# Kernel optimization log

Measured on AMD Instinct MI355X. Metric: run time of the kernel, lower is better.

The kernel has to match this reference:

```python
import jax, jax.numpy as jnp
import numpy as np


def _lstm_cell(x, h, c, Wih, Whh, bih, bhh):
    # PyTorch LSTMCell: gates ordered i, f, g, o
    g = x @ Wih.T + h @ Whh.T + bih + bhh
    H = h.shape[-1]
    i = jax.nn.sigmoid(g[:, :H])
    f = jax.nn.sigmoid(g[:, H:2 * H])
    gg = jnp.tanh(g[:, 2 * H:3 * H])
    o = jax.nn.sigmoid(g[:, 3 * H:])
    c_new = f * c + i * gg
    h_new = o * jnp.tanh(c_new)
    return h_new, c_new


def setup_inputs() -> dict:
    B, S, H = 32, 512, 256
    key = jax.random.key(0)
    ks = jax.random.split(key, 16)
    p = lambda k, shape: jax.random.normal(k, shape, jnp.float32) * 0.05
    return {
        "enc_hidden_states": jax.random.normal(ks[0], (B, S, H), jnp.float32),
        "backward_hidden_state": jax.random.normal(ks[1], (B, H), jnp.float32),
        "backward_cell_state": jax.random.normal(ks[2], (B, H), jnp.float32),
        "attn_W": p(ks[3], (H, 2 * H)),
        "attn_b": p(ks[4], (H,)),
        "attn_V": jax.random.normal(ks[5], (H,), jnp.float32) * 0.1,
        "l1_Wih": p(ks[6], (4 * H, 2 * H)),
        "l1_Whh": p(ks[7], (4 * H, H)),
        "l1_bih": p(ks[8], (4 * H,)),
        "l1_bhh": p(ks[9], (4 * H,)),
        "l2_Wih": p(ks[10], (4 * H, 2 * H)),
        "l2_Whh": p(ks[11], (4 * H, H)),
        "l2_bih": p(ks[12], (4 * H,)),
        "l2_bhh": p(ks[13], (4 * H,)),
        "inp_len": jnp.clip(jax.random.randint(ks[14], (32,), 1, 513), 1, 512).astype(jnp.int32),
    }


def reference(enc_hidden_states, backward_hidden_state, backward_cell_state,
              attn_W, attn_b, attn_V,
              l1_Wih, l1_Whh, l1_bih, l1_bhh,
              l2_Wih, l2_Whh, l2_bih, l2_bhh,
              inp_len):
    B, S, H = enc_hidden_states.shape
    NEG = jnp.float32(-1e9)
    mask = jnp.where(jnp.arange(S)[None, :] < inp_len[:, None], 0.0, NEG)  # (B,S)

    # Linear(cat(q, v)) == q @ Wq.T + v @ Wv.T + b ; hoist out of the time loop.
    Wq, Wv = attn_W[:, :H], attn_W[:, H:]
    pq = enc_hidden_states @ Wq.T                       # (B,S,H)
    pv = enc_hidden_states @ Wv.T + attn_b              # (B,S,H)

    enc_t = jnp.transpose(enc_hidden_states, (1, 0, 2))  # (S,B,H)
    pq_t = jnp.transpose(pq, (1, 0, 2))                   # (S,B,H)

    def step1(carry, xs):
        h, c = carry
        q, pqt = xs
        score = jnp.tanh(pqt[:, None, :] + pv)            # (B,S,H)
        s = jnp.einsum('bsh,h->bs', score, attn_V) + mask
        a = jax.nn.softmax(s, axis=1)
        ctx = jnp.einsum('bs,bsh->bh', a, enc_hidden_states)
        inp = jnp.concatenate([q, ctx], axis=1)           # (B,2H)
        # NOTE: original code passes (decoder_c, decoder_h) i.e. (h=c, c=h) swapped
        h_new, c_new = _lstm_cell(inp, c, h, l1_Wih, l1_Whh, l1_bih, l1_bhh)
        return (h_new, c_new), (h_new, ctx)

    _, (dec_h, ctxs) = jax.lax.scan(step1, (backward_hidden_state, backward_cell_state), (enc_t, pq_t))
    x2 = jnp.concatenate([dec_h, ctxs], axis=2)           # (S,B,2H); dropout = identity (eval)

    # Second layer: packed-sequence LSTM == freeze state and emit zeros past inp_len
    def step2(carry, xs):
        h, c = carry
        x, t = xs
        valid = (t < inp_len)[:, None]
        h_new, c_new = _lstm_cell(x, h, c, l2_Wih, l2_Whh, l2_bih, l2_bhh)
        h2 = jnp.where(valid, h_new, h)
        c2 = jnp.where(valid, c_new, c)
        out = jnp.where(valid, h_new, 0.0)
        return (h2, c2), out

    z = jnp.zeros((B, H), jnp.float32)
    _, out = jax.lax.scan(step2, (z, z), (x2, jnp.arange(S)))
    return jnp.transpose(out, (1, 0, 2))                  # (B,S,H)
```

## Files before the change

### kernel.cpp

```cpp
#include <hip/hip_runtime.h>

typedef _Float16 f16;
typedef _Float16 f16x2 __attribute__((ext_vector_type(2)));
typedef _Float16 f16x8 __attribute__((ext_vector_type(8)));
typedef _Float16 f16x4 __attribute__((ext_vector_type(4)));
typedef float f32x4 __attribute__((ext_vector_type(4)));

#define L2E 1.4426950408889634f
#define K2E 2.8853900817779268f

#define O_PQV   0UL
#define O_GIH2C 0UL
#define O_CTX   33554432UL
#define O_ENCF  41943040UL
#define O_GIH1  50331648UL
#define O_DECT  33554432UL
#define O_WQV   92274688UL
#define O_CPUBT 92274688UL
#define O_H2PT  92340224UL
#define O_W1    92536832UL
#define O_W2    93585408UL
#define O_WHH1  94633984UL
#define O_WHH2  95158272UL
#define O_BQV   95682560UL
#define O_B1    95684608UL
#define O_B2    95688704UL
#define O_V2    95692800UL
#define O_SUMV  95693824UL
#define WS_NEED 95776768UL

__device__ __forceinline__ float fast_sigmoid(float x){
  float e = __builtin_amdgcn_exp2f(-L2E * x);
  return __builtin_amdgcn_rcpf(1.f + e);
}
__device__ __forceinline__ float fast_tanh(float x){
  float e = __builtin_amdgcn_exp2f(K2E * x);
  return 1.f - 2.f * __builtin_amdgcn_rcpf(1.f + e);
}

__device__ __forceinline__ void store_tag(void* p, float a, float b, unsigned tag){
  union { unsigned long long u; unsigned w[2]; } v;
  union { unsigned u; f16 h[2]; } d;
  d.h[0] = (f16)a; d.h[1] = (f16)b;
  v.w[0] = d.u; v.w[1] = tag;
  __hip_atomic_store((unsigned long long*)p, v.u, __ATOMIC_RELAXED, __HIP_MEMORY_SCOPE_AGENT);
}
template<int OFF>
__device__ __forceinline__ int4 ld_i4(const char* p){
  int4 r;
  asm volatile("global_load_dwordx4 %0, %1, off offset:%c2 sc0 sc1"
               : "=v"(r) : "v"(p), "i"(OFF) : "memory");
  return r;
}
__device__ __forceinline__ f16x8 mk_frag(int4 r0, int4 r1){
  union { f16x8 f; int i[4]; } u;
  u.i[0] = r0.x; u.i[1] = r0.z; u.i[2] = r1.x; u.i[3] = r1.z;
  return u.f;
}

__global__ __launch_bounds__(256) void prep_kernel(
    const float* __restrict__ attn_W, const float* __restrict__ attn_b, const float* __restrict__ attn_V,
    const float* __restrict__ l1_Wih, const float* __restrict__ l1_Whh,
    const float* __restrict__ l1_bih, const float* __restrict__ l1_bhh,
    const float* __restrict__ l2_Wih, const float* __restrict__ l2_Whh,
    const float* __restrict__ l2_bih, const float* __restrict__ l2_bhh,
    const float* __restrict__ bcs, char* __restrict__ ws)
{
  long gid = (long)blockIdx.x*256 + threadIdx.x;
  if (gid < 131072){
    int j = (int)(gid >> 8), k = (int)(gid & 255);
    float v = (j < 256) ? attn_W[j*512 + k] : attn_W[(j-256)*512 + 256 + k];
    ((f16*)(ws+O_WQV))[gid] = (f16)(K2E * v);
    return;
  }
  gid -= 131072;
  if (gid < 524288){ ((f16*)(ws+O_W1))[gid] = (f16)l1_Wih[gid]; return; }
  gid -= 524288;
  if (gid < 524288){ ((f16*)(ws+O_W2))[gid] = (f16)l2_Wih[gid]; return; }
  gid -= 524288;
  if (gid < 262144){ ((f16*)(ws+O_WHH1))[gid] = (f16)l1_Whh[gid]; return; }
  gid -= 262144;
  if (gid < 262144){ ((f16*)(ws+O_WHH2))[gid] = (f16)l2_Whh[gid]; return; }
  gid -= 262144;
  if (gid < 512){ ((float*)(ws+O_BQV))[gid] = (gid < 256) ? 0.f : K2E*attn_b[gid-256]; return; }
  gid -= 512;
  if (gid < 1024){ ((float*)(ws+O_B1))[gid] = l1_bih[gid] + l1_bhh[gid]; return; }
  gid -= 1024;
  if (gid < 1024){ ((float*)(ws+O_B2))[gid] = l2_bih[gid] + l2_bhh[gid]; return; }
  gid -= 1024;
  if (gid < 256){ ((float*)(ws+O_V2))[gid] = -2.f*attn_V[gid]; return; }
  gid -= 256;
  if (gid == 0){
    float s = 0.f;
    for (int h=0; h<256; h++) s += attn_V[h];
    *((float*)(ws+O_SUMV)) = s;
  }
}

__global__ __launch_bounds__(256) void encf_kernel(const float* __restrict__ enc, char* __restrict__ ws){
  f16* dst = (f16*)(ws + O_ENCF);
  int i = (blockIdx.x*256 + threadIdx.x)*4;
  float4 v = *(const float4*)(enc + i);
  f16x4 o; o[0] = (f16)v.x; o[1] = (f16)v.y; o[2] = (f16)v.z; o[3] = (f16)v.w;
  *(f16x4*)(dst + i) = o;
}

template<bool CF16>
__global__ __launch_bounds__(256) void gemm_nt(const f16* __restrict__ A0, const f16* __restrict__ A1,
     int K0, const f16* __restrict__ B, int ldb, void* __restrict__ Cp, int ldc,
     int K, const float* __restrict__ bias)
{
  __shared__ f16 As[4096];
  __shared__ f16 Bs[4096];
  const int tid = threadIdx.x;
  const int lane = tid & 63;
  const int wave = tid >> 6;
  const int lm = lane & 15, kg = lane >> 4;
  const int mbase = blockIdx.y * 128;
  const int nbase = blockIdx.x * 128;
  const int wm = (wave >> 1) * 64, wn = (wave & 1) * 64;
  f32x4 acc[4][4];
#pragma unroll
  for (int i=0;i<4;i++)
#pragma unroll
    for (int j=0;j<4;j++) acc[i][j] = 0;
  const int r = tid >> 1, seg = tid & 1;
  for (int kc=0; kc<K; kc+=32){
    const f16* Ap = A0; int kk = kc;
    if (A1 && kc >= K0){ Ap = A1; kk = kc - K0; }
    {
      const f16* srcA = Ap + (size_t)(mbase + r)*256 + kk + seg*16;
      f16x8 va0 = *(const f16x8*)(srcA);
      f16x8 va1 = *(const f16x8*)(srcA + 8);
      *(f16x8*)&As[((seg*2+0)*128 + r)*8] = va0;
      *(f16x8*)&As[((seg*2+1)*128 + r)*8] = va1;
      const f16* srcB = B + (size_t)(nbase + r)*ldb + kc + seg*16;
      f16x8 vb0 = *(const f16x8*)(srcB);
      f16x8 vb1 = *(const f16x8*)(srcB + 8);
      *(f16x8*)&Bs[((seg*2+0)*128 + r)*8] = vb0;
      *(f16x8*)&Bs[((seg*2+1)*128 + r)*8] = vb1;
    }
    __syncthreads();
    f16x8 af[4], bfr[4];
#pragma unroll
    for (int i=0;i<4;i++) af[i]  = *(const f16x8*)&As[(kg*128 + wm + i*16 + lm)*8];
#pragma unroll
    for (int j=0;j<4;j++) bfr[j] = *(const f16x8*)&Bs[(kg*128 + wn + j*16 + lm)*8];
#pragma unroll
    for (int i=0;i<4;i++)
#pragma unroll
      for (int j=0;j<4;j++)
        acc[i][j] = __builtin_amdgcn_mfma_f32_16x16x32_f16(af[i], bfr[j], acc[i][j], 0,0,0);
    __syncthreads();
  }
#pragma unroll
  for (int i=0;i<4;i++){
#pragma unroll
    for (int j=0;j<4;j++){
      int col = nbase + wn + j*16 + lm;
      float bv = bias ? bias[col] : 0.f;
#pragma unroll
      for (int rr=0;rr<4;rr++){
        int row = mbase + wm + i*16 + kg*4 + rr;
        float v = acc[i][j][rr] + bv;
        if (CF16) ((f16*)Cp)[(size_t)row*ldc + col] = (f16)v;
        else      ((float*)Cp)[(size_t)row*ldc + col] = v;
      }
    }
  }
}

__global__ __launch_bounds__(256) void score_ctx_kernel(char* __restrict__ ws,
     const float* __restrict__ enc, const int* __restrict__ inp_len)
{
  __shared__ float s_pq[8][260];
  __shared__ float s_pv[32][260];
  __shared__ float s_sc[8][512];
  __shared__ float s_v2[256];
  __shared__ float s_sv[1];
  const int tid = threadIdx.x;
  const int b = blockIdx.y;
  const int t0 = blockIdx.x * 8;
  const float* pqv = (const float*)(ws + O_PQV);
  f16* ctx = (f16*)(ws + O_CTX);
  const int len = inp_len[b];
  {
    int row = tid >> 5, cb = (tid & 31) * 8;
    const float* src = pqv + (size_t)(b*512 + t0 + row)*512 + cb;
    *(float4*)&s_pq[row][cb]   = *(const float4*)(src);
    *(float4*)&s_pq[row][cb+4] = *(const float4*)(src+4);
    s_v2[tid] = ((const float*)(ws + O_V2))[tid];
    if (tid == 0) s_sv[0] = *((const float*)(ws + O_SUMV));
  }
  const int tt = tid >> 5;
  const int ss2 = tid & 31;
  for (int st=0; st<16; st++){
    {
      int row = tid >> 3, cb = (tid & 7) * 32;
      const float* src = pqv + (size_t)(b*512 + st*32 + row)*512 + 256 + cb;
#pragma unroll
      for (int c=0;c<32;c+=4) *(float4*)&s_pv[row][cb+c] = *(const float4*)(src+c);
    }
    __syncthreads();
    float a0=0.f,a1=0.f,a2=0.f,a3=0.f;
#pragma unroll 8
    for (int h=0;h<256;h+=4){
      float4 q = *(const float4*)&s_pq[tt][h];
      float4 p = *(const float4*)&s_pv[ss2][h];
      float4 w = *(const float4*)&s_v2[h];
      float e0 = __builtin_amdgcn_exp2f(q.x+p.x);
      float e1 = __builtin_amdgcn_exp2f(q.y+p.y);
      float e2 = __builtin_amdgcn_exp2f(q.z+p.z);
      float e3 = __builtin_amdgcn_exp2f(q.w+p.w);
      a0 += w.x * __builtin_amdgcn_rcpf(1.f+e0);
      a1 += w.y * __builtin_amdgcn_rcpf(1.f+e1);
      a2 += w.z * __builtin_amdgcn_rcpf(1.f+e2);
      a3 += w.w * __builtin_amdgcn_rcpf(1.f+e3);
    }
    int s = st*32 + ss2;
    float sc = s_sv[0] + ((a0+a1)+(a2+a3));
    if (s >= len) sc = -1.0e9f;
    s_sc[tt][s] = sc;
    __syncthreads();
  }
  {
    float m = -3.0e38f;
#pragma unroll
    for (int k2=0;k2<16;k2++) m = fmaxf(m, s_sc[tt][ss2 + 32*k2]);
#pragma unroll
    for (int off=16; off>=1; off>>=1) m = fmaxf(m, __shfl_xor(m, off, 64));
    float sum = 0.f;
    float ebuf[16];
#pragma unroll
    for (int k2=0;k2<16;k2++){
      float e = __builtin_amdgcn_exp2f((s_sc[tt][ss2+32*k2] - m) * L2E);
      ebuf[k2] = e; sum += e;
    }
#pragma unroll
    for (int off=16; off>=1; off>>=1) sum += __shfl_xor(sum, off, 64);
    float rinv = __builtin_amdgcn_rcpf(sum);
#pragma unroll
    for (int k2=0;k2<16;k2++) s_sc[tt][ss2+32*k2] = ebuf[k2]*rinv;
  }
  __syncthreads();
  float acc[8] = {0,0,0,0,0,0,0,0};
  const int hg = tid & 31;
  for (int st=0; st<16; st++){
    {
      int row = tid >> 3, cb = (tid & 7)*32;
      const float* src = enc + (size_t)(b*512 + st*32 + row)*256 + cb;
#pragma unroll
      for (int c=0;c<32;c+=4) *(float4*)&s_pv[row][cb+c] = *(const float4*)(src+c);
    }
    __syncthreads();
#pragma unroll 4
    for (int si=0; si<32; si++){
      float a = s_sc[tt][st*32+si];
#pragma unroll
      for (int u=0;u<8;u++) acc[u] += a * s_pv[si][hg + 32*u];
    }
    __syncthreads();
  }
#pragma unroll
  for (int u=0;u<8;u++)
    ctx[(size_t)(b*512 + t0 + tt)*256 + hg + 32*u] = (f16)acc[u];
}

__global__ __launch_bounds__(256) void rec_kernel(char* __restrict__ ws,
        const float* __restrict__ bhs, const float* __restrict__ bcs,
        const int* __restrict__ inp_len, float* __restrict__ out)
{
  __shared__ float s_g[4][32][17];
  __shared__ f16x8 s_buf[2048];
  const int tid = threadIdx.x;
  const int lane = tid & 63;
  const int wave = tid >> 6;
  const int lm = lane & 15;
  const int kg = lane >> 4;
  char* cpubt = ws + O_CPUBT;
  char* h2pt  = ws + O_H2PT;
  char* decpt = ws + O_DECT;
  const int b  = tid >> 3;
  const int kp = tid & 7;
  const int kl0 = kp*2, kl1 = kp*2 + 1;
  const int gslot = wave*256 + lane;
  const int fs = kg*32 + lm;

  if (blockIdx.x < 16) {
    const int isl = blockIdx.x;
    const f16* whh1 = (const f16*)(ws + O_WHH1);
    const f16* gih1 = (const f16*)(ws + O_GIH1);
    f16x8 bf[8];
    {
      int j = wave*256 + isl*16 + lm;
#pragma unroll
      for (int kc=0;kc<8;kc++) bf[kc] = *(const f16x8*)(whh1 + j*256 + kc*32 + kg*8);
    }
    float h0 = bhs[b*256 + isl*16 + kl0];
    float h1 = bhs[b*256 + isl*16 + kl1];
    const int kk0 = isl*16 + kl0;
    const int pu = ((kk0>>5)*128 + ((kk0>>3)&3)*32 + b)*32 + ((kk0&7)>>1)*8;
    store_tag(cpubt + 32768 + pu, bcs[b*256 + kk0], bcs[b*256 + kk0 + 1], 1u);
    for (int t=0;t<512;t++){
      const f16* gp = gih1 + (size_t)(b*512 + t)*1024 + isl*16 + kl0;
      f16x2 gv0 = *(const f16x2*)(gp);
      f16x2 gv1 = *(const f16x2*)(gp+256);
      f16x2 gv2 = *(const f16x2*)(gp+512);
      f16x2 gv3 = *(const f16x2*)(gp+768);
      const char* cb = cpubt + (((t+1)&1)<<15);
      const char* pk0 = cb + (size_t)gslot*32;
      const char* pk2 = pk0 + 4096;
      const unsigned want = (unsigned)(t+1);
      int4 r[8];
      while (true){
        r[0] = ld_i4<0>(pk0);    r[1] = ld_i4<16>(pk0);
        r[2] = ld_i4<2048>(pk0); r[3] = ld_i4<2064>(pk0);
        r[4] = ld_i4<0>(pk2);    r[5] = ld_i4<16>(pk2);
        r[6] = ld_i4<2048>(pk2); r[7] = ld_i4<2064>(pk2);
        asm volatile("s_waitcnt vmcnt(0)" ::: "memory");
        __builtin_amdgcn_sched_barrier(0);
        unsigned mn = 0xFFFFFFFFu;
#pragma unroll
        for (int i=0;i<8;i++){
          unsigned t0 = (unsigned)r[i].y, t1 = (unsigned)r[i].w;
          mn = mn < t0 ? mn : t0;
          mn = mn < t1 ? mn : t1;
        }
        if (__all((int)(mn >= want))) break;
      }
      s_buf[gslot]       = mk_frag(r[0], r[1]);
      s_buf[gslot + 64]  = mk_frag(r[2], r[3]);
      s_buf[gslot + 128] = mk_frag(r[4], r[5]);
      s_buf[gslot + 192] = mk_frag(r[6], r[7]);
      __syncthreads();
      f32x4 acc0 = 0, acc1 = 0;
#pragma unroll
      for (int kc=0;kc<8;kc++){
        f16x8 a0 = s_buf[kc*128 + fs];
        f16x8 a1 = s_buf[kc*128 + fs + 16];
        acc0 = __builtin_amdgcn_mfma_f32_16x16x32_f16(a0, bf[kc], acc0, 0,0,0);
        acc1 = __builtin_amdgcn_mfma_f32_16x16x32_f16(a1, bf[kc], acc1, 0,0,0);
      }
#pragma unroll
      for (int rr=0;rr<4;rr++){
        s_g[wave][kg*4+rr][lm] = acc0[rr];
        s_g[wave][16+kg*4+rr][lm] = acc1[rr];
      }
      __syncthreads();
      {
        float gi0 = s_g[0][b][kl0] + (float)gv0[0];
        float gi1 = s_g[0][b][kl1] + (float)gv0[1];
        float gf0 = s_g[1][b][kl0] + (float)gv1[0];
        float gf1 = s_g[1][b][kl1] + (float)gv1[1];
        float gc0 = s_g[2][b][kl0] + (float)gv2[0];
        float gc1 = s_g[2][b][kl1] + (float)gv2[1];
        float go0 = s_g[3][b][kl0] + (float)gv3[0];
        float go1 = s_g[3][b][kl1] + (float)gv3[1];
        float cn0 = fast_sigmoid(gf0)*h0 + fast_sigmoid(gi0)*fast_tanh(gc0);
        float cn1 = fast_sigmoid(gf1)*h1 + fast_sigmoid(gi1)*fast_tanh(gc1);
        float hn0 = fast_sigmoid(go0)*fast_tanh(cn0);
        float hn1 = fast_sigmoid(go1)*fast_tanh(cn1);
        h0 = hn0; h1 = hn1;
        store_tag(cpubt + ((t&1)<<15) + pu, cn0, cn1, (unsigned)(t+2));
        store_tag(decpt + ((size_t)t<<15) + pu, hn0, hn1, (unsigned)(t+2));
      }
    }
  } else {
    const int isl = blockIdx.x - 16;
    const f16* whh2 = (const f16*)(ws + O_WHH2);
    const f16* w2   = (const f16*)(ws + O_W2);
    const f16* gih2 = (const f16*)(ws + O_GIH2C);
    f16x8 bfh[8], bfx[8];
    {
      int j = wave*256 + isl*16 + lm;
#pragma unroll
      for (int kc=0;kc<8;kc++){
        bfh[kc] = *(const f16x8*)(whh2 + j*256 + kc*32 + kg*8);
        bfx[kc] = *(const f16x8*)(w2 + j*512 + kc*32 + kg*8);
      }
    }
    float c0 = 0.f, c1 = 0.f, hh0 = 0.f, hh1 = 0.f;
    const int lenv = inp_len[b];
    const int kk0 = isl*16 + kl0;
    const int pu = ((kk0>>5)*128 + ((kk0>>3)&3)*32 + b)*32 + ((kk0&7)>>1)*8;
    store_tag(h2pt + 32768 + pu, 0.f, 0.f, 1u);
    for (int t=0;t<512;t++){
      const f16* gp = gih2 + (size_t)(b*512 + t)*1024 + isl*16 + kl0;
      f16x2 gv0 = *(const f16x2*)(gp);
      f16x2 gv1 = *(const f16x2*)(gp+256);
      f16x2 gv2 = *(const f16x2*)(gp+512);
      f16x2 gv3 = *(const f16x2*)(gp+768);
      f32x4 acc0 = 0, acc1 = 0;
      {
        const char* xb = decpt + ((size_t)t<<15);
        const char* px0 = xb + (size_t)gslot*32;
        const char* px2 = px0 + 4096;
        const unsigned wantx = (unsigned)(t+2);
        int4 rx[8];
        while (true){
          rx[0] = ld_i4<0>(px0);    rx[1] = ld_i4<16>(px0);
          rx[2] = ld_i4<2048>(px0); rx[3] = ld_i4<2064>(px0);
          rx[4] = ld_i4<0>(px2);    rx[5] = ld_i4<16>(px2);
          rx[6] = ld_i4<2048>(px2); rx[7] = ld_i4<2064>(px2);
          asm volatile("s_waitcnt vmcnt(0)" ::: "memory");
          __builtin_amdgcn_sched_barrier(0);
          unsigned mn = 0xFFFFFFFFu;
#pragma unroll
          for (int i=0;i<8;i++){
            unsigned a0 = (unsigned)rx[i].y, a1 = (unsigned)rx[i].w;
            mn = mn < a0 ? mn : a0;
            mn = mn < a1 ? mn : a1;
          }
          if (__all((int)(mn >= wantx))) break;
        }
        s_buf[gslot]       = mk_frag(rx[0], rx[1]);
        s_buf[gslot + 64]  = mk_frag(rx[2], rx[3]);
        s_buf[gslot + 128] = mk_frag(rx[4], rx[5]);
        s_buf[gslot + 192] = mk_frag(rx[6], rx[7]);
      }
      __syncthreads();
#pragma unroll
      for (int kc=0;kc<8;kc++){
        f16x8 ax0 = s_buf[kc*128 + fs];
        f16x8 ax1 = s_buf[kc*128 + fs + 16];
        acc0 = __builtin_amdgcn_mfma_f32_16x16x32_f16(ax0, bfx[kc], acc0, 0,0,0);
        acc1 = __builtin_amdgcn_mfma_f32_16x16x32_f16(ax1, bfx[kc], acc1, 0,0,0);
      }
      {
        const char* hb = h2pt + (((t+1)&1)<<15);
        const char* ph0 = hb + (size_t)gslot*32;
        const char* ph2 = ph0 + 4096;
        const unsigned wanth = (unsigned)(t+1);
        int4 rh[8];
        while (true){
          rh[0] = ld_i4<0>(ph0);    rh[1] = ld_i4<16>(ph0);
          rh[2] = ld_i4<2048>(ph0); rh[3] = ld_i4<2064>(ph0);
          rh[4] = ld_i4<0>(ph2);    rh[5] = ld_i4<16>(ph2);
          rh[6] = ld_i4<2048>(ph2); rh[7] = ld_i4<2064>(ph2);
          asm volatile("s_waitcnt vmcnt(0)" ::: "memory");
          __builtin_amdgcn_sched_barrier(0);
          unsigned mn = 0xFFFFFFFFu;
#pragma unroll
          for (int i=0;i<8;i++){
            unsigned b0 = (unsigned)rh[i].y, b1 = (unsigned)rh[i].w;
            mn = mn < b0 ? mn : b0;
            mn = mn < b1 ? mn : b1;
          }
          if (__all((int)(mn >= wanth))) break;
        }
        s_buf[1024 + gslot]       = mk_frag(rh[0], rh[1]);
        s_buf[1024 + gslot + 64]  = mk_frag(rh[2], rh[3]);
        s_buf[1024 + gslot + 128] = mk_frag(rh[4], rh[5]);
        s_buf[1024 + gslot + 192] = mk_frag(rh[6], rh[7]);
      }
      __syncthreads();
#pragma unroll
      for (int kc=0;kc<8;kc++){
        f16x8 ah0 = s_buf[1024 + kc*128 + fs];
        f16x8 ah1 = s_buf[1024 + kc*128 + fs + 16];
        acc0 = __builtin_amdgcn_mfma_f32_16x16x32_f16(ah0, bfh[kc], acc0, 0,0,0);
        acc1 = __builtin_amdgcn_mfma_f32_16x16x32_f16(ah1, bfh[kc], acc1, 0,0,0);
      }
#pragma unroll
      for (int rr=0;rr<4;rr++){
        s_g[wave][kg*4+rr][lm] = acc0[rr];
        s_g[wave][16+kg*4+rr][lm] = acc1[rr];
      }
      __syncthreads();
      float ov0, ov1;
      {
        float gi0 = s_g[0][b][kl0] + (float)gv0[0];
        float gi1 = s_g[0][b][kl1] + (float)gv0[1];
        float gf0 = s_g[1][b][kl0] + (float)gv1[0];
        float gf1 = s_g[1][b][kl1] + (float)gv1[1];
        float gc0 = s_g[2][b][kl0] + (float)gv2[0];
        float gc1 = s_g[2][b][kl1] + (float)gv2[1];
        float go0 = s_g[3][b][kl0] + (float)gv3[0];
        float go1 = s_g[3][b][kl1] + (float)gv3[1];
        float cn0 = fast_sigmoid(gf0)*c0 + fast_sigmoid(gi0)*fast_tanh(gc0);
        float cn1 = fast_sigmoid(gf1)*c1 + fast_sigmoid(gi1)*fast_tanh(gc1);
        float hn0 = fast_sigmoid(go0)*fast_tanh(cn0);
        float hn1 = fast_sigmoid(go1)*fast_tanh(cn1);
        bool valid = (t < lenv);
        c0 = valid ? cn0 : c0;
        c1 = valid ? cn1 : c1;
        hh0 = valid ? hn0 : hh0;
        hh1 = valid ? hn1 : hh1;
        ov0 = valid ? hn0 : 0.f;
        ov1 = valid ? hn1 : 0.f;
        store_tag(h2pt + ((t&1)<<15) + pu, hh0, hh1, (unsigned)(t+2));
      }
      float2 ov; ov.x = ov0; ov.y = ov1;
      *(float2*)(out + (size_t)(b*512 + t)*256 + isl*16 + kl0) = ov;
    }
  }
}

extern "C" void kernel_launch(void* const* d_in, const int* in_sizes, int n_in,
                              void* d_out, int out_size, void* d_ws, size_t ws_size,
                              hipStream_t stream) {
  if (ws_size < WS_NEED) return;
  const float* enc    = (const float*)d_in[0];
  const float* bhs    = (const float*)d_in[1];
  const float* bcs    = (const float*)d_in[2];
  const float* attn_W = (const float*)d_in[3];
  const float* attn_b = (const float*)d_in[4];
  const float* attn_V = (const float*)d_in[5];
  const float* l1_Wih = (const float*)d_in[6];
  const float* l1_Whh = (const float*)d_in[7];
  const float* l1_bih = (const float*)d_in[8];
  const float* l1_bhh = (const float*)d_in[9];
  const float* l2_Wih = (const float*)d_in[10];
  const float* l2_Whh = (const float*)d_in[11];
  const float* l2_bih = (const float*)d_in[12];
  const float* l2_bhh = (const float*)d_in[13];
  const int* inp_len  = (const int*)d_in[14];
  char* ws = (char*)d_ws;
  float* out = (float*)d_out;

  prep_kernel<<<6700, 256, 0, stream>>>(attn_W, attn_b, attn_V, l1_Wih, l1_Whh, l1_bih, l1_bhh,
                                        l2_Wih, l2_Whh, l2_bih, l2_bhh, bcs, ws);
  encf_kernel<<<4096, 256, 0, stream>>>(enc, ws);
  gemm_nt<false><<<dim3(4,128), 256, 0, stream>>>((const f16*)(ws+O_ENCF), nullptr, 256,
        (const f16*)(ws+O_WQV), 256, (void*)(ws+O_PQV), 512, 256, (const float*)(ws+O_BQV));
  score_ctx_kernel<<<dim3(64,32), 256, 0, stream>>>(ws, enc, inp_len);
  gemm_nt<true><<<dim3(8,128), 256, 0, stream>>>((const f16*)(ws+O_ENCF), (const f16*)(ws+O_CTX), 256,
        (const f16*)(ws+O_W1), 512, (void*)(ws+O_GIH1), 1024, 512, (const float*)(ws+O_B1));
  gemm_nt<true><<<dim3(8,128), 256, 0, stream>>>((const f16*)(ws+O_CTX), nullptr, 256,
        (const f16*)(ws+O_W2)+256, 512, (void*)(ws+O_GIH2C), 1024, 256, (const float*)(ws+O_B2));
  hipMemsetAsync(ws + O_DECT, 0, 16777216UL, stream);
  hipMemsetAsync(ws + O_CPUBT, 0, 131072UL, stream);
  rec_kernel<<<32, 256, 0, stream>>>(ws, bhs, bcs, inp_len, out);
}
```

Baseline: 2.350 ms.

## Skip padded attention chunks and pipeline layer-2 input projection one step ahead

The score/softmax/context kernel now loops only over the 32-wide sequence chunks that cover inp_len for each batch row, skipping fully masked positions. In the layer-2 recurrent loop, the wait on the decoder-output tag, the gate-input load and the input-projection MFMAs for step t+1 now run after step t finishes, not at the start of each step. This is meant to take x-side work off the h-dependency critical path. It adds a dynamic loop bound, drops unrolling of the softmax loops, and relies on the moved spin-wait ordering staying deadlock free.

Measured after the change: 2.083 ms. 1.13x faster.

```diff
diff --git a/kernel.cpp b/kernel.cpp
--- a/kernel.cpp
+++ b/kernel.cpp
@@ -184,6 +184,7 @@
   const float* pqv = (const float*)(ws + O_PQV);
   f16* ctx = (f16*)(ws + O_CTX);
   const int len = inp_len[b];
+  const int stmax = (len + 31) >> 5;
   {
     int row = tid >> 5, cb = (tid & 31) * 8;
     const float* src = pqv + (size_t)(b*512 + t0 + row)*512 + cb;
@@ -194,7 +195,7 @@
   }
   const int tt = tid >> 5;
   const int ss2 = tid & 31;
-  for (int st=0; st<16; st++){
+  for (int st=0; st<stmax; st++){
     {
       int row = tid >> 3, cb = (tid & 7) * 32;
       const float* src = pqv + (size_t)(b*512 + st*32 + row)*512 + 256 + cb;
@@ -225,27 +226,24 @@
   }
   {
     float m = -3.0e38f;
-#pragma unroll
-    for (int k2=0;k2<16;k2++) m = fmaxf(m, s_sc[tt][ss2 + 32*k2]);
+    for (int k2=0;k2<stmax;k2++) m = fmaxf(m, s_sc[tt][ss2 + 32*k2]);
 #pragma unroll
     for (int off=16; off>=1; off>>=1) m = fmaxf(m, __shfl_xor(m, off, 64));
     float sum = 0.f;
     float ebuf[16];
-#pragma unroll
-    for (int k2=0;k2<16;k2++){
+    for (int k2=0;k2<stmax;k2++){
       float e = __builtin_amdgcn_exp2f((s_sc[tt][ss2+32*k2] - m) * L2E);
       ebuf[k2] = e; sum += e;
     }
 #pragma unroll
     for (int off=16; off>=1; off>>=1) sum += __shfl_xor(sum, off, 64);
     float rinv = __builtin_amdgcn_rcpf(sum);
-#pragma unroll
-    for (int k2=0;k2<16;k2++) s_sc[tt][ss2+32*k2] = ebuf[k2]*rinv;
+    for (int k2=0;k2<stmax;k2++) s_sc[tt][ss2+32*k2] = ebuf[k2]*rinv;
   }
   __syncthreads();
   float acc[8] = {0,0,0,0,0,0,0,0};
   const int hg = tid & 31;
-  for (int st=0; st<16; st++){
+  for (int st=0; st<stmax; st++){
     {
       int row = tid >> 3, cb = (tid & 7)*32;
       const float* src = enc + (size_t)(b*512 + st*32 + row)*256 + cb;
@@ -384,40 +382,37 @@
     const int kk0 = isl*16 + kl0;
     const int pu = ((kk0>>5)*128 + ((kk0>>3)&3)*32 + b)*32 + ((kk0&7)>>1)*8;
     store_tag(h2pt + 32768 + pu, 0.f, 0.f, 1u);
-    for (int t=0;t<512;t++){
-      const f16* gp = gih2 + (size_t)(b*512 + t)*1024 + isl*16 + kl0;
-      f16x2 gv0 = *(const f16x2*)(gp);
-      f16x2 gv1 = *(const f16x2*)(gp+256);
-      f16x2 gv2 = *(const f16x2*)(gp+512);
-      f16x2 gv3 = *(const f16x2*)(gp+768);
-      f32x4 acc0 = 0, acc1 = 0;
-      {
-        const char* xb = decpt + ((size_t)t<<15);
-        const char* px0 = xb + (size_t)gslot*32;
-        const char* px2 = px0 + 4096;
-        const unsigned wantx = (unsigned)(t+2);
-        int4 rx[8];
-        while (true){
-          rx[0] = ld_i4<0>(px0);    rx[1] = ld_i4<16>(px0);
-          rx[2] = ld_i4<2048>(px0); rx[3] = ld_i4<2064>(px0);
-          rx[4] = ld_i4<0>(px2);    rx[5] = ld_i4<16>(px2);
-          rx[6] = ld_i4<2048>(px2); rx[7] = ld_i4<2064>(px2);
-          asm volatile("s_waitcnt vmcnt(0)" ::: "memory");
-          __builtin_amdgcn_sched_barrier(0);
-          unsigned mn = 0xFFFFFFFFu;
-#pragma unroll
-          for (int i=0;i<8;i++){
-            unsigned a0 = (unsigned)rx[i].y, a1 = (unsigned)rx[i].w;
-            mn = mn < a0 ? mn : a0;
-            mn = mn < a1 ? mn : a1;
-          }
-          if (__all((int)(mn >= wantx))) break;
+    f16x2 gv0, gv1, gv2, gv3;
+    f32x4 acc0 = 0, acc1 = 0;
+    {
+      const f16* gp = gih2 + (size_t)(b*512)*1024 + isl*16 + kl0;
+      gv0 = *(const f16x2*)(gp);
+      gv1 = *(const f16x2*)(gp+256);
+      gv2 = *(const f16x2*)(gp+512);
+      gv3 = *(const f16x2*)(gp+768);
+      const char* px0 = decpt + (size_t)gslot*32;
+      const char* px2 = px0 + 4096;
+      int4 rx[8];
+      while (true){
+        rx[0] = ld_i4<0>(px0);    rx[1] = ld_i4<16>(px0);
+        rx[2] = ld_i4<2048>(px0); rx[3] = ld_i4<2064>(px0);
+        rx[4] = ld_i4<0>(px2);    rx[5] = ld_i4<16>(px2);
+        rx[6] = ld_i4<2048>(px2); rx[7] = ld_i4<2064>(px2);
+        asm volatile("s_waitcnt vmcnt(0)" ::: "memory");
+        __builtin_amdgcn_sched_barrier(0);
+        unsigned mn = 0xFFFFFFFFu;
+#pragma unroll
+        for (int i=0;i<8;i++){
+          unsigned a0 = (unsigned)rx[i].y, a1 = (unsigned)rx[i].w;
+          mn = mn < a0 ? mn : a0;
+          mn = mn < a1 ? mn : a1;
         }
-        s_buf[gslot]       = mk_frag(rx[0], rx[1]);
-        s_buf[gslot + 64]  = mk_frag(rx[2], rx[3]);
-        s_buf[gslot + 128] = mk_frag(rx[4], rx[5]);
-        s_buf[gslot + 192] = mk_frag(rx[6], rx[7]);
-      }
+        if (__all((int)(mn >= 2u))) break;
+      }
+      s_buf[gslot]       = mk_frag(rx[0], rx[1]);
+      s_buf[gslot + 64]  = mk_frag(rx[2], rx[3]);
+      s_buf[gslot + 128] = mk_frag(rx[4], rx[5]);
+      s_buf[gslot + 192] = mk_frag(rx[6], rx[7]);
       __syncthreads();
 #pragma unroll
       for (int kc=0;kc<8;kc++){
@@ -426,6 +421,8 @@
         acc0 = __builtin_amdgcn_mfma_f32_16x16x32_f16(ax0, bfx[kc], acc0, 0,0,0);
         acc1 = __builtin_amdgcn_mfma_f32_16x16x32_f16(ax1, bfx[kc], acc1, 0,0,0);
       }
+    }
+    for (int t=0;t<512;t++){
       {
         const char* hb = h2pt + (((t+1)&1)<<15);
         const char* ph0 = hb + (size_t)gslot*32;
@@ -492,6 +489,47 @@
       }
       float2 ov; ov.x = ov0; ov.y = ov1;
       *(float2*)(out + (size_t)(b*512 + t)*256 + isl*16 + kl0) = ov;
+      if (t < 511){
+        const f16* gp = gih2 + (size_t)(b*512 + (t+1))*1024 + isl*16 + kl0;
+        gv0 = *(const f16x2*)(gp);
+        gv1 = *(const f16x2*)(gp+256);
+        gv2 = *(const f16x2*)(gp+512);
+        gv3 = *(const f16x2*)(gp+768);
+        const char* xb = decpt + ((size_t)(t+1)<<15);
+        const char* px0 = xb + (size_t)gslot*32;
+        const char* px2 = px0 + 4096;
+        const unsigned wantx = (unsigned)(t+3);
+        int4 rx[8];
+        while (true){
+          rx[0] = ld_i4<0>(px0);    rx[1] = ld_i4<16>(px0);
+          rx[2] = ld_i4<2048>(px0); rx[3] = ld_i4<2064>(px0);
+          rx[4] = ld_i4<0>(px2);    rx[5] = ld_i4<16>(px2);
+          rx[6] = ld_i4<2048>(px2); rx[7] = ld_i4<2064>(px2);
+          asm volatile("s_waitcnt vmcnt(0)" ::: "memory");
+          __builtin_amdgcn_sched_barrier(0);
+          unsigned mn = 0xFFFFFFFFu;
+#pragma unroll
+          for (int i=0;i<8;i++){
+            unsigned a0 = (unsigned)rx[i].y, a1 = (unsigned)rx[i].w;
+            mn = mn < a0 ? mn : a0;
+            mn = mn < a1 ? mn : a1;
+          }
+          if (__all((int)(mn >= wantx))) break;
+        }
+        s_buf[gslot]       = mk_frag(rx[0], rx[1]);
+        s_buf[gslot + 64]  = mk_frag(rx[2], rx[3]);
+        s_buf[gslot + 128] = mk_frag(rx[4], rx[5]);
+        s_buf[gslot + 192] = mk_frag(rx[6], rx[7]);
+        __syncthreads();
+        acc0 = 0; acc1 = 0;
+#pragma unroll
+        for (int kc=0;kc<8;kc++){
+          f16x8 ax0 = s_buf[kc*128 + fs];
+          f16x8 ax1 = s_buf[kc*128 + fs + 16];
+          acc0 = __builtin_amdgcn_mfma_f32_16x16x32_f16(ax0, bfx[kc], acc0, 0,0,0);
+          acc1 = __builtin_amdgcn_mfma_f32_16x16x32_f16(ax1, bfx[kc], acc1, 0,0,0);
+        }
+      }
     }
   }
 }
```
